# Optimization experiments

Measured on AMD Instinct MI355X. Metric: run time of the kernel, lower is better.

The kernel has to match this reference:

```python
import jax, jax.numpy as jnp
import numpy as np

NODE_DIM = 64
OUT_DIM = 64
EDGE_DIM = 64
N_NODES = 50000
N_EDGES = 800000
BN_EPS = 1e-5


def _batchnorm(x, gamma, beta):
    # training-mode BatchNorm1d: biased batch statistics
    mean = jnp.mean(x, axis=0)
    var = jnp.mean((x - mean) ** 2, axis=0)
    return (x - mean) * jax.lax.rsqrt(var + BN_EPS) * gamma + beta


def setup_inputs() -> dict:
    key = jax.random.key(0)
    ks = jax.random.split(key, 16)
    s = 0.05  # weight init scale
    inp = {
        "em": jax.random.normal(ks[0], (N_NODES, NODE_DIM), jnp.float32),
        "edge_index": jax.random.randint(ks[1], (2, N_EDGES), 0, N_NODES, jnp.int64),
        "edge_features": jax.random.normal(ks[2], (N_EDGES, EDGE_DIM), jnp.float32),
        # GINEConv edge linear (edge_dim -> node_dim)
        "W_le": jax.random.normal(ks[3], (EDGE_DIM, NODE_DIM), jnp.float32) * s,
        "b_le": jnp.zeros((NODE_DIM,), jnp.float32),
        # GINEConv nn: Linear(node_dim, out) -> ReLU -> Linear(out, out)
        "W1": jax.random.normal(ks[4], (NODE_DIM, OUT_DIM), jnp.float32) * s,
        "b1": jnp.zeros((OUT_DIM,), jnp.float32),
        "W2": jax.random.normal(ks[5], (OUT_DIM, OUT_DIM), jnp.float32) * s,
        "b2": jnp.zeros((OUT_DIM,), jnp.float32),
        # x BatchNorm affine
        "gx": jnp.ones((OUT_DIM,), jnp.float32),
        "bx": jnp.zeros((OUT_DIM,), jnp.float32),
        # edge MLP: (edge_dim + 2*out) -> out -> out -> out
        "We1": jax.random.normal(ks[6], (EDGE_DIM + 2 * OUT_DIM, OUT_DIM), jnp.float32) * s,
        "be1": jnp.zeros((OUT_DIM,), jnp.float32),
        "We2": jax.random.normal(ks[7], (OUT_DIM, OUT_DIM), jnp.float32) * s,
        "be2": jnp.zeros((OUT_DIM,), jnp.float32),
        "We3": jax.random.normal(ks[8], (OUT_DIM, OUT_DIM), jnp.float32) * s,
        "be3": jnp.zeros((OUT_DIM,), jnp.float32),
        # edge BatchNorm affine
        "ge": jnp.ones((OUT_DIM,), jnp.float32),
        "be": jnp.zeros((OUT_DIM,), jnp.float32),
    }
    return inp


def reference(em, edge_index, edge_features, W_le, b_le, W1, b1, W2, b2, gx, bx,
              We1, be1, We2, be2, We3, be3, ge, be):
    src, dst = edge_index[0], edge_index[1]
    # GINEConv: msg = relu(x_j + lin(edge_attr)), sum-aggregated at target
    msg = jax.nn.relu(em[src] + edge_features @ W_le + b_le)  # [E, node_dim]
    aggr = jax.ops.segment_sum(msg, dst, num_segments=em.shape[0])  # [N, node_dim]
    h = em + aggr  # eps = 0
    h = jax.nn.relu(h @ W1 + b1) @ W2 + b2  # [N, out]
    x_em = jax.nn.relu(_batchnorm(h, gx, bx))
    # edge update: concat(x_em[src], x_em[dst], edge_features)
    edge_mess = jnp.concatenate([x_em[src], x_em[dst], edge_features], axis=1)
    e = jax.nn.relu(edge_mess @ We1 + be1)
    e = jax.nn.relu(e @ We2 + be2)
    e = e @ We3 + be3
    edge_out = jax.nn.relu(_batchnorm(e, ge, be))
    return x_em, edge_out
```

## Files before the change

kernel.cpp:

```cpp
#include <hip/hip_runtime.h>
#include <cstddef>
#include <cstdint>

#define NN 50000
#define NE 800000

typedef __bf16 bf16x8 __attribute__((ext_vector_type(8)));
typedef float  f32x4  __attribute__((ext_vector_type(4)));

__device__ __forceinline__ bf16x8 ldfrag(const __bf16* __restrict__ wfr, int f, int lane) {
    return *reinterpret_cast<const bf16x8*>(wfr + (size_t)(f * 64 + lane) * 8);
}
__device__ __forceinline__ f32x4 mfma16(bf16x8 a, bf16x8 b, f32x4 c) {
    return __builtin_amdgcn_mfma_f32_16x16x32_bf16(a, b, c, 0, 0, 0);
}
__device__ __forceinline__ bool idx_is64(const int* eidx) {
    return ((eidx[1] | eidx[3] | eidx[5] | eidx[7]) == 0);
}
__device__ __forceinline__ int ld_src(const int* eidx, bool is64, int e) {
    return is64 ? eidx[(size_t)2 * e] : eidx[e];
}
__device__ __forceinline__ int ld_dst(const int* eidx, bool is64, int e) {
    return is64 ? eidx[2 * ((size_t)NE + e)] : eidx[(size_t)NE + e];
}
__device__ __forceinline__ bf16x8 cvt8(const float* __restrict__ p) {
    float4 v0 = *reinterpret_cast<const float4*>(p);
    float4 v1 = *reinterpret_cast<const float4*>(p + 4);
    bf16x8 r;
    r[0] = (__bf16)v0.x; r[1] = (__bf16)v0.y; r[2] = (__bf16)v0.z; r[3] = (__bf16)v0.w;
    r[4] = (__bf16)v1.x; r[5] = (__bf16)v1.y; r[6] = (__bf16)v1.z; r[7] = (__bf16)v1.w;
    return r;
}

__global__ __launch_bounds__(256) void prep(const float* __restrict__ wle, const float* __restrict__ w1,
                                            const float* __restrict__ w2, const float* __restrict__ we1,
                                            const float* __restrict__ we2, const float* __restrict__ we3,
                                            __bf16* __restrict__ wfr, float* __restrict__ sums) {
    if (blockIdx.x == 0) sums[threadIdx.x] = 0.f;
    int sid = blockIdx.x * 256 + threadIdx.x;
    int f = sid >> 6, lane = sid & 63;
    const float* W; int fo;
    if (f < 8)       { W = wle; fo = 0; }
    else if (f < 16) { W = w1;  fo = 8; }
    else if (f < 24) { W = w2;  fo = 16; }
    else if (f < 48) { W = we1; fo = 24; }
    else if (f < 56) { W = we2; fo = 48; }
    else             { W = we3; fo = 56; }
    int lf = f - fo, kt = lf >> 2, nt = lf & 3;
    int g = lane >> 4, c = lane & 15;
#pragma unroll
    for (int b = 0; b < 8; b++) {
        int k = kt * 32 + g * 8 + b;
        int n = nt * 16 + c;
        wfr[(size_t)(f * 64 + lane) * 8 + b] = (__bf16)W[(size_t)k * 64 + n];
    }
}

__global__ __launch_bounds__(256) void k1(const float* __restrict__ em, const int* __restrict__ eidx,
                                          const float* __restrict__ ef, const __bf16* __restrict__ wfr,
                                          const float* __restrict__ ble, float* __restrict__ nodebuf) {
    __shared__ __bf16 Ash[64][72];
    const int t = threadIdx.x;
    const int base = blockIdx.x * 64;
    {
        const int r = t >> 2, seg = t & 3;
        const float4* p = reinterpret_cast<const float4*>(ef + (size_t)(base + r) * 64 + seg * 16);
#pragma unroll
        for (int i = 0; i < 4; i++) {
            float4 v = p[i];
            int cb = seg * 16 + i * 4;
            Ash[r][cb + 0] = (__bf16)v.x; Ash[r][cb + 1] = (__bf16)v.y;
            Ash[r][cb + 2] = (__bf16)v.z; Ash[r][cb + 3] = (__bf16)v.w;
        }
    }
    const bool is64 = idx_is64(eidx);
    __syncthreads();
    const int lane = t & 63, w = t >> 6, c = lane & 15, g = lane >> 4;
    const int arow = w * 16 + c;
    f32x4 acc[4] = {{0.f,0.f,0.f,0.f},{0.f,0.f,0.f,0.f},{0.f,0.f,0.f,0.f},{0.f,0.f,0.f,0.f}};
#pragma unroll
    for (int kt = 0; kt < 2; kt++) {
        bf16x8 a = *reinterpret_cast<const bf16x8*>(&Ash[arow][kt * 32 + g * 8]);
#pragma unroll
        for (int nt = 0; nt < 4; nt++) acc[nt] = mfma16(a, ldfrag(wfr, kt * 4 + nt, lane), acc[nt]);
    }
#pragma unroll
    for (int rr = 0; rr < 4; rr++) {
        int e = base + w * 16 + g * 4 + rr;
        int sn = ld_src(eidx, is64, e);
        int dn = ld_dst(eidx, is64, e);
#pragma unroll
        for (int nt = 0; nt < 4; nt++) {
            int col = nt * 16 + c;
            float v = acc[nt][rr] + ble[col] + em[(size_t)sn * 64 + col];
            if (v > 0.f) atomicAdd(&nodebuf[(size_t)dn * 64 + col], v);
        }
    }
}

__global__ __launch_bounds__(256) void k2(const float* __restrict__ em, float* __restrict__ nb,
                                          const __bf16* __restrict__ wfr, const float* __restrict__ b1,
                                          const float* __restrict__ b2, float* __restrict__ sums) {
    __shared__ __bf16 Ysh[64][72];
    __shared__ float bs[128];
    const int t = threadIdx.x;
    const int base = blockIdx.x * 64;
    if (t < 128) bs[t] = 0.f;
    __syncthreads();
    const int lane = t & 63, w = t >> 6, c = lane & 15, g = lane >> 4;
    const int arow = base + w * 16 + c;
    const size_t rl = (size_t)(arow < NN ? arow : NN - 1) * 64;
    bf16x8 a[2];
#pragma unroll
    for (int kt = 0; kt < 2; kt++) {
        int off = kt * 32 + g * 8;
        float4 e0 = *reinterpret_cast<const float4*>(em + rl + off);
        float4 e1 = *reinterpret_cast<const float4*>(em + rl + off + 4);
        float4 n0 = *reinterpret_cast<const float4*>(nb + rl + off);
        float4 n1 = *reinterpret_cast<const float4*>(nb + rl + off + 4);
        bf16x8 r;
        r[0] = (__bf16)(e0.x + n0.x); r[1] = (__bf16)(e0.y + n0.y);
        r[2] = (__bf16)(e0.z + n0.z); r[3] = (__bf16)(e0.w + n0.w);
        r[4] = (__bf16)(e1.x + n1.x); r[5] = (__bf16)(e1.y + n1.y);
        r[6] = (__bf16)(e1.z + n1.z); r[7] = (__bf16)(e1.w + n1.w);
        a[kt] = r;
    }
    f32x4 a1[4] = {{0.f,0.f,0.f,0.f},{0.f,0.f,0.f,0.f},{0.f,0.f,0.f,0.f},{0.f,0.f,0.f,0.f}};
#pragma unroll
    for (int kt = 0; kt < 2; kt++)
#pragma unroll
        for (int nt = 0; nt < 4; nt++) a1[nt] = mfma16(a[kt], ldfrag(wfr, 8 + kt * 4 + nt, lane), a1[nt]);
#pragma unroll
    for (int nt = 0; nt < 4; nt++) {
        float bb = b1[nt * 16 + c];
#pragma unroll
        for (int rr = 0; rr < 4; rr++) {
            float v = a1[nt][rr] + bb;
            v = v > 0.f ? v : 0.f;
            Ysh[w * 16 + g * 4 + rr][nt * 16 + c] = (__bf16)v;
        }
    }
    bf16x8 ya[2];
#pragma unroll
    for (int kt = 0; kt < 2; kt++)
        ya[kt] = *reinterpret_cast<const bf16x8*>(&Ysh[w * 16 + c][kt * 32 + g * 8]);
    f32x4 a2[4] = {{0.f,0.f,0.f,0.f},{0.f,0.f,0.f,0.f},{0.f,0.f,0.f,0.f},{0.f,0.f,0.f,0.f}};
#pragma unroll
    for (int kt = 0; kt < 2; kt++)
#pragma unroll
        for (int nt = 0; nt < 4; nt++) a2[nt] = mfma16(ya[kt], ldfrag(wfr, 16 + kt * 4 + nt, lane), a2[nt]);
#pragma unroll
    for (int nt = 0; nt < 4; nt++) {
        int col = nt * 16 + c;
        float bb = b2[col];
        float ss = 0.f, qq = 0.f;
#pragma unroll
        for (int rr = 0; rr < 4; rr++) {
            int row = base + w * 16 + g * 4 + rr;
            if (row < NN) {
                float v = a2[nt][rr] + bb;
                nb[(size_t)row * 64 + col] = v;
                ss += v; qq += v * v;
            }
        }
        ss += __shfl_xor(ss, 16); ss += __shfl_xor(ss, 32);
        qq += __shfl_xor(qq, 16); qq += __shfl_xor(qq, 32);
        if (g == 0) { atomicAdd(&bs[col], ss); atomicAdd(&bs[64 + col], qq); }
    }
    __syncthreads();
    if (t < 128) atomicAdd(&sums[t], bs[t]);
}

__global__ __launch_bounds__(256) void k3(float* __restrict__ nb, const float* __restrict__ sums,
                                          const float* __restrict__ gx, const float* __restrict__ bx,
                                          __bf16* __restrict__ wsx) {
    size_t i4 = (size_t)(blockIdx.x * 256 + threadIdx.x) * 4;
    int col0 = (int)(i4 & 63);
    float4 v = *reinterpret_cast<const float4*>(nb + i4);
    const float* pv = reinterpret_cast<const float*>(&v);
    float o[4]; short so[4];
#pragma unroll
    for (int j = 0; j < 4; j++) {
        int col = col0 + j;
        float m   = sums[col] * (1.0f / 50000.0f);
        float var = sums[64 + col] * (1.0f / 50000.0f) - m * m;
        float inv = rsqrtf(var + 1e-5f);
        float x = (pv[j] - m) * inv * gx[col] + bx[col];
        x = x > 0.f ? x : 0.f;
        o[j] = x;
        so[j] = __builtin_bit_cast(short, (__bf16)x);
    }
    *reinterpret_cast<float4*>(nb + i4) = make_float4(o[0], o[1], o[2], o[3]);
    *reinterpret_cast<short4*>(wsx + i4) = make_short4(so[0], so[1], so[2], so[3]);
}

__global__ __launch_bounds__(256) void k4(const int* __restrict__ eidx, const float* __restrict__ ef,
                                          const __bf16* __restrict__ wsx, const __bf16* __restrict__ wfr,
                                          const float* __restrict__ be1, const float* __restrict__ be2,
                                          const float* __restrict__ be3, float* __restrict__ eout,
                                          float* __restrict__ pws) {
    __shared__ __bf16 Ysh[2][64][72];
    __shared__ float bs[128];
    const int t = threadIdx.x;
    const int blockb = blockIdx.x * 128;
    if (t < 128) bs[t] = 0.f;
    __syncthreads();
    const int lane = t & 63, w = t >> 6, c = lane & 15, g = lane >> 4;
    const bool is64 = idx_is64(eidx);

    int erow[2], sn[2], dn[2];
    bf16x8 xs[2][2], xd[2][2], ea[2][2];
#pragma unroll
    for (int tt = 0; tt < 2; tt++) {
        erow[tt] = blockb + tt * 64 + w * 16 + c;
        sn[tt] = ld_src(eidx, is64, erow[tt]);
        dn[tt] = ld_dst(eidx, is64, erow[tt]);
#pragma unroll
        for (int kt = 0; kt < 2; kt++) {
            int off = kt * 32 + g * 8;
            xs[tt][kt] = *reinterpret_cast<const bf16x8*>(wsx + (size_t)sn[tt] * 64 + off);
            xd[tt][kt] = *reinterpret_cast<const bf16x8*>(wsx + (size_t)dn[tt] * 64 + off);
            ea[tt][kt] = cvt8(ef + (size_t)erow[tt] * 64 + off);
        }
    }
    f32x4 a1[2][4];
#pragma unroll
    for (int tt = 0; tt < 2; tt++)
#pragma unroll
        for (int nt = 0; nt < 4; nt++) a1[tt][nt] = f32x4{0.f,0.f,0.f,0.f};
    __builtin_amdgcn_s_setprio(1);
#pragma unroll
    for (int tt = 0; tt < 2; tt++)
#pragma unroll
        for (int kt = 0; kt < 2; kt++)
#pragma unroll
            for (int nt = 0; nt < 4; nt++) a1[tt][nt] = mfma16(xs[tt][kt], ldfrag(wfr, 24 + kt * 4 + nt, lane), a1[tt][nt]);
#pragma unroll
    for (int tt = 0; tt < 2; tt++)
#pragma unroll
        for (int kt = 0; kt < 2; kt++)
#pragma unroll
            for (int nt = 0; nt < 4; nt++) a1[tt][nt] = mfma16(xd[tt][kt], ldfrag(wfr, 32 + kt * 4 + nt, lane), a1[tt][nt]);
#pragma unroll
    for (int tt = 0; tt < 2; tt++)
#pragma unroll
        for (int kt = 0; kt < 2; kt++)
#pragma unroll
            for (int nt = 0; nt < 4; nt++) a1[tt][nt] = mfma16(ea[tt][kt], ldfrag(wfr, 40 + kt * 4 + nt, lane), a1[tt][nt]);
    __builtin_amdgcn_s_setprio(0);
#pragma unroll
    for (int tt = 0; tt < 2; tt++)
#pragma unroll
        for (int nt = 0; nt < 4; nt++) {
            float bb = be1[nt * 16 + c];
#pragma unroll
            for (int rr = 0; rr < 4; rr++) {
                float v = a1[tt][nt][rr] + bb;
                v = v > 0.f ? v : 0.f;
                Ysh[tt][w * 16 + g * 4 + rr][nt * 16 + c] = (__bf16)v;
            }
        }
    bf16x8 ya[2][2];
#pragma unroll
    for (int tt = 0; tt < 2; tt++)
#pragma unroll
        for (int kt = 0; kt < 2; kt++)
            ya[tt][kt] = *reinterpret_cast<const bf16x8*>(&Ysh[tt][w * 16 + c][kt * 32 + g * 8]);
    f32x4 a2[2][4];
#pragma unroll
    for (int tt = 0; tt < 2; tt++)
#pragma unroll
        for (int nt = 0; nt < 4; nt++) a2[tt][nt] = f32x4{0.f,0.f,0.f,0.f};
    __builtin_amdgcn_s_setprio(1);
#pragma unroll
    for (int tt = 0; tt < 2; tt++)
#pragma unroll
        for (int kt = 0; kt < 2; kt++)
#pragma unroll
            for (int nt = 0; nt < 4; nt++) a2[tt][nt] = mfma16(ya[tt][kt], ldfrag(wfr, 48 + kt * 4 + nt, lane), a2[tt][nt]);
    __builtin_amdgcn_s_setprio(0);
#pragma unroll
    for (int tt = 0; tt < 2; tt++)
#pragma unroll
        for (int nt = 0; nt < 4; nt++) {
            float bb = be2[nt * 16 + c];
#pragma unroll
            for (int rr = 0; rr < 4; rr++) {
                float v = a2[tt][nt][rr] + bb;
                v = v > 0.f ? v : 0.f;
                Ysh[tt][w * 16 + g * 4 + rr][nt * 16 + c] = (__bf16)v;
            }
        }
#pragma unroll
    for (int tt = 0; tt < 2; tt++)
#pragma unroll
        for (int kt = 0; kt < 2; kt++)
            ya[tt][kt] = *reinterpret_cast<const bf16x8*>(&Ysh[tt][w * 16 + c][kt * 32 + g * 8]);
    f32x4 a3[2][4];
#pragma unroll
    for (int tt = 0; tt < 2; tt++)
#pragma unroll
        for (int nt = 0; nt < 4; nt++) a3[tt][nt] = f32x4{0.f,0.f,0.f,0.f};
    __builtin_amdgcn_s_setprio(1);
#pragma unroll
    for (int tt = 0; tt < 2; tt++)
#pragma unroll
        for (int kt = 0; kt < 2; kt++)
#pragma unroll
            for (int nt = 0; nt < 4; nt++) a3[tt][nt] = mfma16(ya[tt][kt], ldfrag(wfr, 56 + kt * 4 + nt, lane), a3[tt][nt]);
    __builtin_amdgcn_s_setprio(0);
#pragma unroll
    for (int tt = 0; tt < 2; tt++)
#pragma unroll
        for (int nt = 0; nt < 4; nt++) {
            int col = nt * 16 + c;
            float bb = be3[col];
            float ss = 0.f, qq = 0.f;
#pragma unroll
            for (int rr = 0; rr < 4; rr++) {
                int e = blockb + tt * 64 + w * 16 + g * 4 + rr;
                float v = a3[tt][nt][rr] + bb;
                __builtin_nontemporal_store(v, &eout[(size_t)e * 64 + col]);
                ss += v; qq += v * v;
            }
            ss += __shfl_xor(ss, 16); ss += __shfl_xor(ss, 32);
            qq += __shfl_xor(qq, 16); qq += __shfl_xor(qq, 32);
            if (g == 0) { atomicAdd(&bs[col], ss); atomicAdd(&bs[64 + col], qq); }
        }
    __syncthreads();
    if (t < 128) pws[(size_t)t * (NE / 128) + blockIdx.x] = bs[t];
}

__global__ __launch_bounds__(256) void k4r(const float* __restrict__ pws, float* __restrict__ sums) {
    int b = blockIdx.x;
    float s = 0.f;
    for (int i = threadIdx.x; i < NE / 128; i += 256) s += pws[(size_t)b * (NE / 128) + i];
#pragma unroll
    for (int m = 32; m >= 1; m >>= 1) s += __shfl_xor(s, m);
    __shared__ float acc4[4];
    int lane = threadIdx.x & 63, wid = threadIdx.x >> 6;
    if (lane == 0) acc4[wid] = s;
    __syncthreads();
    if (threadIdx.x == 0) sums[128 + b] = acc4[0] + acc4[1] + acc4[2] + acc4[3];
}

__global__ __launch_bounds__(256) void k5(float* __restrict__ eo, const float* __restrict__ sums,
                                          const float* __restrict__ ge, const float* __restrict__ be) {
    __shared__ float sc[64], sh[64];
    if (threadIdx.x < 64) {
        int col = threadIdx.x;
        float m   = sums[128 + col] * (1.0f / 800000.0f);
        float var = sums[192 + col] * (1.0f / 800000.0f) - m * m;
        float inv = rsqrtf(var + 1e-5f) * ge[col];
        sc[col] = inv;
        sh[col] = be[col] - m * inv;
    }
    __syncthreads();
    const size_t total = (size_t)NE * 64 / 4;
    for (size_t i = (size_t)blockIdx.x * 256 + threadIdx.x; i < total; i += (size_t)gridDim.x * 256) {
        f32x4 v = __builtin_nontemporal_load(reinterpret_cast<const f32x4*>(eo) + i);
        int col0 = (int)((i * 4) & 63);
        f32x4 o;
#pragma unroll
        for (int j = 0; j < 4; j++) {
            float x = v[j] * sc[col0 + j] + sh[col0 + j];
            o[j] = x > 0.f ? x : 0.f;
        }
        __builtin_nontemporal_store(o, reinterpret_cast<f32x4*>(eo) + i);
    }
}

extern "C" void kernel_launch(void* const* d_in, const int* in_sizes, int n_in,
                              void* d_out, int out_size, void* d_ws, size_t ws_size,
                              hipStream_t stream) {
    const float* em   = (const float*)d_in[0];
    const int*   eidx = (const int*)d_in[1];
    const float* ef   = (const float*)d_in[2];
    const float* b_le = (const float*)d_in[4];
    const float* b1   = (const float*)d_in[6];
    const float* b2   = (const float*)d_in[8];
    const float* gx   = (const float*)d_in[9];
    const float* bx   = (const float*)d_in[10];
    const float* be1  = (const float*)d_in[12];
    const float* be2  = (const float*)d_in[14];
    const float* be3  = (const float*)d_in[16];
    const float* ge   = (const float*)d_in[17];
    const float* be   = (const float*)d_in[18];

    float* out = (float*)d_out;
    float* nodebuf = out;
    float* eout = out + (size_t)NN * 64;

    float*  sums = (float*)d_ws;
    __bf16* wfr  = (__bf16*)((char*)d_ws + 1024);
    __bf16* wsx  = (__bf16*)((char*)d_ws + 1024 + 65536);
    float*  pws  = (float*)((char*)d_ws + 1024 + 65536 + (size_t)NN * 64 * 2);

    hipMemsetAsync(nodebuf, 0, (size_t)NN * 64 * sizeof(float), stream);

    prep<<<16, 256, 0, stream>>>((const float*)d_in[3], (const float*)d_in[5], (const float*)d_in[7],
                                 (const float*)d_in[11], (const float*)d_in[13], (const float*)d_in[15],
                                 wfr, sums);
    k1<<<NE / 64, 256, 0, stream>>>(em, eidx, ef, wfr, b_le, nodebuf);
    k2<<<(NN + 63) / 64, 256, 0, stream>>>(em, nodebuf, wfr, b1, b2, sums);
    k3<<<(NN * 64) / 1024, 256, 0, stream>>>(nodebuf, sums, gx, bx, wsx);
    k4<<<NE / 128, 256, 0, stream>>>(eidx, ef, wsx, wfr, be1, be2, be3, eout, pws);
    k4r<<<128, 256, 0, stream>>>(pws, sums);
    k5<<<2048, 256, 0, stream>>>(eout, sums, ge, be);
}
```

Baseline: 443.3 us.

## Split scatter-add into column-group-major aggregation buffers across 4x more blocks

The edge message kernel is split so each block handles one 16-column group of a 64-edge tile, launching four times as many blocks. Atomics go into a column-group-major workspace buffer (4 x NN x 16), so each group's atomic target region is a quarter the size and more likely to stay cache-resident. The node MLP kernel now reads aggregates from this layout instead of the output buffer. The cost is that each edge-feature tile is loaded and converted four times and index loads are repeated per block, in exchange for more parallelism and better atomic locality.

```diff
diff --git a/kernel.cpp b/kernel.cpp
--- a/kernel.cpp
+++ b/kernel.cpp
@@ -58,10 +58,12 @@
 
 __global__ __launch_bounds__(256) void k1(const float* __restrict__ em, const int* __restrict__ eidx,
                                           const float* __restrict__ ef, const __bf16* __restrict__ wfr,
-                                          const float* __restrict__ ble, float* __restrict__ nodebuf) {
+                                          const float* __restrict__ ble, float* __restrict__ aggrcg) {
     __shared__ __bf16 Ash[64][72];
     const int t = threadIdx.x;
-    const int base = blockIdx.x * 64;
+    const int tile = blockIdx.x >> 2;
+    const int cg   = blockIdx.x & 3;
+    const int base = tile * 64;
     {
         const int r = t >> 2, seg = t & 3;
         const float4* p = reinterpret_cast<const float4*>(ef + (size_t)(base + r) * 64 + seg * 16);
@@ -77,30 +79,28 @@
     __syncthreads();
     const int lane = t & 63, w = t >> 6, c = lane & 15, g = lane >> 4;
     const int arow = w * 16 + c;
-    f32x4 acc[4] = {{0.f,0.f,0.f,0.f},{0.f,0.f,0.f,0.f},{0.f,0.f,0.f,0.f},{0.f,0.f,0.f,0.f}};
+    const int col = cg * 16 + c;
+    f32x4 acc = {0.f, 0.f, 0.f, 0.f};
 #pragma unroll
     for (int kt = 0; kt < 2; kt++) {
         bf16x8 a = *reinterpret_cast<const bf16x8*>(&Ash[arow][kt * 32 + g * 8]);
-#pragma unroll
-        for (int nt = 0; nt < 4; nt++) acc[nt] = mfma16(a, ldfrag(wfr, kt * 4 + nt, lane), acc[nt]);
-    }
+        acc = mfma16(a, ldfrag(wfr, kt * 4 + cg, lane), acc);
+    }
+    const float bb = ble[col];
 #pragma unroll
     for (int rr = 0; rr < 4; rr++) {
         int e = base + w * 16 + g * 4 + rr;
         int sn = ld_src(eidx, is64, e);
         int dn = ld_dst(eidx, is64, e);
-#pragma unroll
-        for (int nt = 0; nt < 4; nt++) {
-            int col = nt * 16 + c;
-            float v = acc[nt][rr] + ble[col] + em[(size_t)sn * 64 + col];
-            if (v > 0.f) atomicAdd(&nodebuf[(size_t)dn * 64 + col], v);
-        }
-    }
-}
-
-__global__ __launch_bounds__(256) void k2(const float* __restrict__ em, float* __restrict__ nb,
-                                          const __bf16* __restrict__ wfr, const float* __restrict__ b1,
-                                          const float* __restrict__ b2, float* __restrict__ sums) {
+        float v = acc[rr] + bb + em[(size_t)sn * 64 + col];
+        if (v > 0.f) atomicAdd(&aggrcg[((size_t)cg * NN + dn) * 16 + c], v);
+    }
+}
+
+__global__ __launch_bounds__(256) void k2(const float* __restrict__ em, const float* __restrict__ aggrcg,
+                                          float* __restrict__ nb, const __bf16* __restrict__ wfr,
+                                          const float* __restrict__ b1, const float* __restrict__ b2,
+                                          float* __restrict__ sums) {
     __shared__ __bf16 Ysh[64][72];
     __shared__ float bs[128];
     const int t = threadIdx.x;
@@ -109,15 +109,17 @@
     __syncthreads();
     const int lane = t & 63, w = t >> 6, c = lane & 15, g = lane >> 4;
     const int arow = base + w * 16 + c;
-    const size_t rl = (size_t)(arow < NN ? arow : NN - 1) * 64;
+    const int rowc = arow < NN ? arow : NN - 1;
+    const size_t rl = (size_t)rowc * 64;
     bf16x8 a[2];
 #pragma unroll
     for (int kt = 0; kt < 2; kt++) {
         int off = kt * 32 + g * 8;
+        const float* pa = aggrcg + ((size_t)(off >> 4) * NN + rowc) * 16 + (off & 15);
         float4 e0 = *reinterpret_cast<const float4*>(em + rl + off);
         float4 e1 = *reinterpret_cast<const float4*>(em + rl + off + 4);
-        float4 n0 = *reinterpret_cast<const float4*>(nb + rl + off);
-        float4 n1 = *reinterpret_cast<const float4*>(nb + rl + off + 4);
+        float4 n0 = *reinterpret_cast<const float4*>(pa);
+        float4 n1 = *reinterpret_cast<const float4*>(pa + 4);
         bf16x8 r;
         r[0] = (__bf16)(e0.x + n0.x); r[1] = (__bf16)(e0.y + n0.y);
         r[2] = (__bf16)(e0.z + n0.z); r[3] = (__bf16)(e0.w + n0.w);
@@ -391,18 +393,20 @@
     float* nodebuf = out;
     float* eout = out + (size_t)NN * 64;
 
-    float*  sums = (float*)d_ws;
-    __bf16* wfr  = (__bf16*)((char*)d_ws + 1024);
-    __bf16* wsx  = (__bf16*)((char*)d_ws + 1024 + 65536);
-    float*  pws  = (float*)((char*)d_ws + 1024 + 65536 + (size_t)NN * 64 * 2);
-
-    hipMemsetAsync(nodebuf, 0, (size_t)NN * 64 * sizeof(float), stream);
+    char* wsb = (char*)d_ws;
+    float*  sums   = (float*)wsb;
+    __bf16* wfr    = (__bf16*)(wsb + 1024);
+    __bf16* wsx    = (__bf16*)(wsb + 1024 + 65536);
+    float*  pws    = (float*)(wsb + 1024 + 65536 + (size_t)NN * 64 * 2);
+    float*  aggrcg = (float*)(wsb + 1024 + 65536 + (size_t)NN * 64 * 2 + (size_t)128 * (NE / 128) * 4);
+
+    hipMemsetAsync(aggrcg, 0, (size_t)4 * NN * 16 * sizeof(float), stream);
 
     prep<<<16, 256, 0, stream>>>((const float*)d_in[3], (const float*)d_in[5], (const float*)d_in[7],
                                  (const float*)d_in[11], (const float*)d_in[13], (const float*)d_in[15],
                                  wfr, sums);
-    k1<<<NE / 64, 256, 0, stream>>>(em, eidx, ef, wfr, b_le, nodebuf);
-    k2<<<(NN + 63) / 64, 256, 0, stream>>>(em, nodebuf, wfr, b1, b2, sums);
+    k1<<<(NE / 64) * 4, 256, 0, stream>>>(em, eidx, ef, wfr, b_le, aggrcg);
+    k2<<<(NN + 63) / 64, 256, 0, stream>>>(em, aggrcg, nodebuf, wfr, b1, b2, sums);
     k3<<<(NN * 64) / 1024, 256, 0, stream>>>(nodebuf, sums, gx, bx, wsx);
     k4<<<NE / 128, 256, 0, stream>>>(eidx, ef, wsx, wfr, be1, be2, be3, eout, pws);
     k4r<<<128, 256, 0, stream>>>(pws, sums);
```

New measurement: 477.2 us. 1.08x slower.
